# Kernel optimization log

Hardware: AMD Instinct MI355X
Metric: run time of the kernel (lower is better)

Reference implementation:

```python
import jax, jax.numpy as jnp
import numpy as np

SE_W, SE_H = 3, 3  # se_size

def _unfold_blocks(x):
    # x: (B, C, W, H) -> (B, C, w*h, W, H), replicating torch pad+unfold+view flat layout
    B, C, W, H = x.shape
    pw, ph = SE_W // 2, SE_H // 2
    x_pad = jnp.pad(x, ((0, 0), (0, 0), (pw, pw), (ph, ph)))
    # stack 9 shifted views; flat order (b,c,wi,hi,k) matches torch (B,C,1,W,H,w,h)
    blocks = jnp.stack(
        [x_pad[:, :, i:i + W, j:j + H] for i in range(SE_W) for j in range(SE_H)],
        axis=-1,
    )  # (B, C, W, H, 9)
    # torch: .view(B, C, w*h, 1, W, H).squeeze(3) -> flat reinterpretation, not a transpose
    return blocks.reshape(B, C, SE_W * SE_H, W, H)


def setup_inputs() -> dict:
    key = jax.random.key(0)
    k1, k2, k3, k4 = jax.random.split(key, 4)
    B, C, W, H = 8, 128, 64, 64
    x = jax.random.normal(k1, (B, C, W, H), dtype=jnp.float32)
    se_param = jax.random.normal(k2, (SE_W * SE_H,), dtype=jnp.float32)
    # Conv3d(channels, channels, kernel_size=1): weight (O, C, 1, 1, 1) -> (O, C)
    bound = 1.0 / np.sqrt(C)
    attn_w = jax.random.uniform(k3, (C, C), dtype=jnp.float32, minval=-bound, maxval=bound)
    attn_b = jax.random.uniform(k4, (C,), dtype=jnp.float32, minval=-bound, maxval=bound)
    return {"x": x, "se_param": se_param, "attn_w": attn_w, "attn_b": attn_b}


def reference(x, se_param, attn_w, attn_b):
    se = jax.nn.sigmoid(se_param)                      # (9,)
    blocks = _unfold_blocks(x)                          # (B, C, 9, W, H)
    weighted = blocks * se[None, None, :, None, None]   # (B, C, 9, W, H)
    # pointwise Conv3d over channel dim (same weight at every (s, w, h) position)
    mixed = jnp.einsum('bcswh,oc->boswh', weighted, attn_w) \
        + attn_b[None, :, None, None, None]
    attn = jax.nn.sigmoid(mixed)
    out = jnp.max(weighted * attn, axis=2)              # (B, C, W, H)
    return out
```

## Files before the change

kernel.cpp:

```cpp
#include <hip/hip_runtime.h>

#define CCH 128
#define SP  4096
#define BROWS 10
#define RSTR 76
#define BSZ2 (BROWS * RSTR)
#define GOFF 16
#define GTOT (GOFF + 9 * BSZ2)
#define T16_OFF 65536
#define TBLK 80
#define XTSTR 136
#define LOG2E 1.4426950408889634f

typedef __attribute__((ext_vector_type(8))) short bf16x8;
typedef __attribute__((ext_vector_type(4))) float f32x4;

__device__ __forceinline__ float sigmoidf_(float z) {
  return 1.0f / (1.0f + __expf(-z));
}

__device__ __forceinline__ unsigned short bf16rne(float f) {
  union { float f; unsigned u; } v; v.f = f;
  return (unsigned short)((v.u + 0x7fffu + ((v.u >> 16) & 1u)) >> 16);
}

__device__ __forceinline__ int tap_off(int s, int wh) {
  int q  = (s << 12) + wh;
  int wi = q / 576;  int r  = q - wi * 576;
  int hi = r / 9;    int kk = r - hi * 9;
  int di = kk / 3,   dj = kk - di * 3;
  int sw = wi + di - 1, sh = hi + dj - 1;
  bool valid = ((unsigned)sw < 64u) & ((unsigned)sh < 64u);
  int wilo = (s * 64) / 9;
  int rb = sw - wilo + 1;
  return valid ? (GOFF + s * BSZ2 + rb * RSTR + sh) : 0;
}

template <bool WS>
__global__ __launch_bounds__(256) void k_conv(
    const float* __restrict__ x, const float* __restrict__ attn_w,
    float* __restrict__ y, unsigned* __restrict__ t32,
    unsigned short* __restrict__ t16) {
  int bid = blockIdx.x;
  if (WS) {
    if (bid < TBLK) {
      int i = bid * 256 + threadIdx.x;
      if (i < 4 * SP) {
        int wh = i >> 2, j = i & 3;
        unsigned lo = (unsigned)tap_off(2 * j, wh);
        unsigned hi = (unsigned)tap_off(2 * j + 1, wh);
        t32[i] = lo | (hi << 16);
      } else if (i < 5 * SP) {
        int wh = i & (SP - 1);
        t16[wh] = (unsigned short)tap_off(8, wh);
      }
      return;
    }
    bid -= TBLK;
  }

  __shared__ unsigned short x_t[32 * XTSTR];

  int b  = bid >> 7;
  int nb = bid & 127;
  int lane = threadIdx.x & 63, wv = threadIdx.x >> 6;

  const float* xpb = x + ((size_t)b << 19) + (nb << 5);
  int n_st  = threadIdx.x & 31;
  int c_st  = (threadIdx.x >> 5) << 2;
  float xv[16];
#pragma unroll
  for (int g = 0; g < 4; g++) {
    int c0 = c_st + (g << 5);
#pragma unroll
    for (int i = 0; i < 4; i++)
      xv[g * 4 + i] = xpb[((size_t)(c0 + i) << 12) + n_st];
  }

  bf16x8 afrag[2][4];
#pragma unroll
  for (int ot = 0; ot < 2; ot++)
#pragma unroll
    for (int ks = 0; ks < 4; ks++) {
      int o = (wv << 5) + (ot << 4) + (lane & 15);
      int k = (ks << 5) + ((lane >> 4) << 3);
      const float4* wp = (const float4*)&attn_w[(o << 7) + k];
      float4 a0 = wp[0], a1 = wp[1];
      bf16x8 f;
      f[0] = (short)bf16rne(a0.x); f[1] = (short)bf16rne(a0.y);
      f[2] = (short)bf16rne(a0.z); f[3] = (short)bf16rne(a0.w);
      f[4] = (short)bf16rne(a1.x); f[5] = (short)bf16rne(a1.y);
      f[6] = (short)bf16rne(a1.z); f[7] = (short)bf16rne(a1.w);
      afrag[ot][ks] = f;
    }

#pragma unroll
  for (int g = 0; g < 4; g++) {
    int c0 = c_st + (g << 5);
    union { unsigned short s[2]; unsigned u; } p0, p1;
    p0.s[0] = bf16rne(xv[g * 4 + 0]); p0.s[1] = bf16rne(xv[g * 4 + 1]);
    p1.s[0] = bf16rne(xv[g * 4 + 2]); p1.s[1] = bf16rne(xv[g * 4 + 3]);
    *(uint2*)&x_t[n_st * XTSTR + c0] = make_uint2(p0.u, p1.u);
  }
  __syncthreads();

  f32x4 acc[2][2] = {};
#pragma unroll
  for (int ks = 0; ks < 4; ks++) {
    bf16x8 bfrag[2];
#pragma unroll
    for (int nt = 0; nt < 2; nt++) {
      int n = (nt << 4) + (lane & 15);
      int k = (ks << 5) + ((lane >> 4) << 3);
      bfrag[nt] = *(const bf16x8*)&x_t[n * XTSTR + k];
    }
#pragma unroll
    for (int ot = 0; ot < 2; ot++)
#pragma unroll
      for (int nt = 0; nt < 2; nt++)
        acc[ot][nt] = __builtin_amdgcn_mfma_f32_16x16x32_bf16(
            afrag[ot][ks], bfrag[nt], acc[ot][nt], 0, 0, 0);
  }

  float* yb = y + ((size_t)b << 19) + (nb << 5);
#pragma unroll
  for (int ot = 0; ot < 2; ot++) {
    int ob = (wv << 5) + (ot << 4) + ((lane >> 4) << 2);
#pragma unroll
    for (int nt = 0; nt < 2; nt++) {
      int n = (nt << 4) + (lane & 15);
#pragma unroll
      for (int r = 0; r < 4; r++)
        yb[((size_t)(ob + r) << 12) + n] = acc[ot][nt][r];
    }
  }
}

template <bool TBL>
__global__ __launch_bounds__(256) void k_attnmax(
    const float* __restrict__ x, float* __restrict__ yo,
    const float* __restrict__ se_param, const float* __restrict__ attn_b,
    const uint4* __restrict__ t32, const unsigned short* __restrict__ t16) {
  __shared__ float g[GTOT];
  __shared__ float se9[16];
  __shared__ float sl9[16];

  int bc = blockIdx.x;
  int c  = bc & (CCH - 1);
  const float* xp = x  + ((size_t)bc << 12);
  float*       yp = yo + ((size_t)bc << 12);

  if (threadIdx.x < 9) {
    float se = sigmoidf_(se_param[threadIdx.x]);
    se9[threadIdx.x] = se;
    sl9[threadIdx.x] = -se * LOG2E;
  }
  if (threadIdx.x == 0) g[0] = 0.0f;
  float ab = attn_b[c];
  float abl = -ab * LOG2E;
  __syncthreads();

  for (int f = threadIdx.x; f < 9 * BROWS * 16; f += 256) {
    int s   = f / 160;
    int rem = f - s * 160;
    int rb  = rem >> 4, sh0 = (rem & 15) << 2;
    int rg  = ((s * 64 * 58255) >> 19) - 1 + rb;
    float4 gv = make_float4(0.0f, 0.0f, 0.0f, 0.0f);
    if ((unsigned)rg < 64u) {
      float se = se9[s], sl = sl9[s];
      float4 xx = *(const float4*)&xp[(rg << 6) + sh0];
      float4 yy = *(const float4*)&yp[(rg << 6) + sh0];
      gv.x = se * xx.x * __builtin_amdgcn_rcpf(1.0f + exp2f(fmaf(yy.x, sl, abl)));
      gv.y = se * xx.y * __builtin_amdgcn_rcpf(1.0f + exp2f(fmaf(yy.y, sl, abl)));
      gv.z = se * xx.z * __builtin_amdgcn_rcpf(1.0f + exp2f(fmaf(yy.z, sl, abl)));
      gv.w = se * xx.w * __builtin_amdgcn_rcpf(1.0f + exp2f(fmaf(yy.w, sl, abl)));
    }
    *(float4*)&g[GOFF + s * BSZ2 + rb * RSTR + sh0] = gv;
  }
  __syncthreads();

  for (int k = 0; k < 16; k++) {
    int wh = (k << 8) | threadIdx.x;
    float m;
    if (TBL) {
      uint4 p = t32[wh];
      int p8  = t16[wh];
      float m0 = fmaxf(g[p.x & 0xffffu], g[p.x >> 16]);
      float m1 = fmaxf(g[p.y & 0xffffu], g[p.y >> 16]);
      float m2 = fmaxf(g[p.z & 0xffffu], g[p.z >> 16]);
      float m3 = fmaxf(g[p.w & 0xffffu], g[p.w >> 16]);
      m = fmaxf(fmaxf(fmaxf(m0, m1), fmaxf(m2, m3)), g[p8]);
    } else {
      m = 0.0f;
#pragma unroll
      for (int s = 0; s < 9; s++) m = fmaxf(m, g[tap_off(s, wh)]);
    }
    yp[wh] = m;
  }
}

extern "C" void kernel_launch(void* const* d_in, const int* in_sizes, int n_in,
                              void* d_out, int out_size, void* d_ws, size_t ws_size,
                              hipStream_t stream) {
  const float* x        = (const float*)d_in[0];
  const float* se_param = (const float*)d_in[1];
  const float* attn_w   = (const float*)d_in[2];
  const float* attn_b   = (const float*)d_in[3];
  float* out = (float*)d_out;

  int B = in_sizes[0] / (CCH * SP);
  unsigned* t32       = (unsigned*)d_ws;
  unsigned short* t16 = (unsigned short*)((char*)d_ws + T16_OFF);
  bool use_ws = ws_size >= (size_t)(T16_OFF + SP * sizeof(unsigned short));

  if (use_ws) {
    k_conv<true><<<dim3(TBLK + B * 128), dim3(256), 0, stream>>>(
        x, attn_w, out, t32, t16);
    k_attnmax<true><<<dim3(B * CCH), dim3(256), 0, stream>>>(
        x, out, se_param, attn_b, (const uint4*)t32, t16);
  } else {
    k_conv<false><<<dim3(B * 128), dim3(256), 0, stream>>>(
        x, attn_w, out, nullptr, nullptr);
    k_attnmax<false><<<dim3(B * CCH), dim3(256), 0, stream>>>(
        x, out, se_param, attn_b, nullptr, nullptr);
  }
}
```

Measured before the change: 30.54 us.

## Store conv intermediate as bf16 in workspace and halve conv tile width

The 1x1 channel-mix result is now written as bf16 into a workspace buffer instead of fp32 into the output, and the attention/max kernel reads bf16 values back. This halves the intermediate write and read traffic. Conv blocks now cover 16 spatial positions instead of 32, which doubles the block count and shrinks per-block LDS and registers. The bf16 rounding of pre-sigmoid logits adds error, and the fast path needs a larger workspace, otherwise the fp32 fallback kernels run.

```diff
diff --git a/kernel.cpp b/kernel.cpp
--- a/kernel.cpp
+++ b/kernel.cpp
@@ -8,6 +8,7 @@
 #define GOFF 16
 #define GTOT (GOFF + 9 * BSZ2)
 #define T16_OFF 65536
+#define Y_OFFB 73728
 #define TBLK 80
 #define XTSTR 136
 #define LOG2E 1.4426950408889634f
@@ -22,6 +23,11 @@
 __device__ __forceinline__ unsigned short bf16rne(float f) {
   union { float f; unsigned u; } v; v.f = f;
   return (unsigned short)((v.u + 0x7fffu + ((v.u >> 16) & 1u)) >> 16);
+}
+
+__device__ __forceinline__ float bf2f(unsigned short u) {
+  union { unsigned u; float f; } v; v.u = (unsigned)u << 16;
+  return v.f;
 }
 
 __device__ __forceinline__ int tap_off(int s, int wh) {
@@ -36,46 +42,39 @@
   return valid ? (GOFF + s * BSZ2 + rb * RSTR + sh) : 0;
 }
 
-template <bool WS>
 __global__ __launch_bounds__(256) void k_conv(
     const float* __restrict__ x, const float* __restrict__ attn_w,
-    float* __restrict__ y, unsigned* __restrict__ t32,
+    unsigned short* __restrict__ ybf, unsigned* __restrict__ t32,
     unsigned short* __restrict__ t16) {
   int bid = blockIdx.x;
-  if (WS) {
-    if (bid < TBLK) {
-      int i = bid * 256 + threadIdx.x;
-      if (i < 4 * SP) {
-        int wh = i >> 2, j = i & 3;
-        unsigned lo = (unsigned)tap_off(2 * j, wh);
-        unsigned hi = (unsigned)tap_off(2 * j + 1, wh);
-        t32[i] = lo | (hi << 16);
-      } else if (i < 5 * SP) {
-        int wh = i & (SP - 1);
-        t16[wh] = (unsigned short)tap_off(8, wh);
-      }
-      return;
-    }
-    bid -= TBLK;
-  }
-
-  __shared__ unsigned short x_t[32 * XTSTR];
-
-  int b  = bid >> 7;
-  int nb = bid & 127;
+  if (bid < TBLK) {
+    int i = bid * 256 + threadIdx.x;
+    if (i < 4 * SP) {
+      int wh = i >> 2, j = i & 3;
+      unsigned lo = (unsigned)tap_off(2 * j, wh);
+      unsigned hi = (unsigned)tap_off(2 * j + 1, wh);
+      t32[i] = lo | (hi << 16);
+    } else if (i < 5 * SP) {
+      int wh = i & (SP - 1);
+      t16[wh] = (unsigned short)tap_off(8, wh);
+    }
+    return;
+  }
+  bid -= TBLK;
+
+  __shared__ unsigned short x_t[16 * XTSTR];
+
+  int b  = bid >> 8;
+  int nb = bid & 255;
   int lane = threadIdx.x & 63, wv = threadIdx.x >> 6;
 
-  const float* xpb = x + ((size_t)b << 19) + (nb << 5);
-  int n_st  = threadIdx.x & 31;
-  int c_st  = (threadIdx.x >> 5) << 2;
-  float xv[16];
-#pragma unroll
-  for (int g = 0; g < 4; g++) {
-    int c0 = c_st + (g << 5);
-#pragma unroll
-    for (int i = 0; i < 4; i++)
-      xv[g * 4 + i] = xpb[((size_t)(c0 + i) << 12) + n_st];
-  }
+  const float* xpb = x + ((size_t)b << 19) + (nb << 4);
+  int n_st = threadIdx.x & 15;
+  int c_st = (threadIdx.x >> 4) << 3;
+  float xv[8];
+#pragma unroll
+  for (int i = 0; i < 8; i++)
+    xv[i] = xpb[((size_t)(c_st + i) << 12) + n_st];
 
   bf16x8 afrag[2][4];
 #pragma unroll
@@ -94,56 +93,158 @@
       afrag[ot][ks] = f;
     }
 
-#pragma unroll
-  for (int g = 0; g < 4; g++) {
-    int c0 = c_st + (g << 5);
-    union { unsigned short s[2]; unsigned u; } p0, p1;
-    p0.s[0] = bf16rne(xv[g * 4 + 0]); p0.s[1] = bf16rne(xv[g * 4 + 1]);
-    p1.s[0] = bf16rne(xv[g * 4 + 2]); p1.s[1] = bf16rne(xv[g * 4 + 3]);
-    *(uint2*)&x_t[n_st * XTSTR + c0] = make_uint2(p0.u, p1.u);
-  }
-  __syncthreads();
-
-  f32x4 acc[2][2] = {};
+  union { unsigned short s[8]; uint4 q; } pk;
+#pragma unroll
+  for (int i = 0; i < 8; i++) pk.s[i] = bf16rne(xv[i]);
+  *(uint4*)&x_t[n_st * XTSTR + c_st] = pk.q;
+  __syncthreads();
+
+  f32x4 acc[2] = {};
 #pragma unroll
   for (int ks = 0; ks < 4; ks++) {
-    bf16x8 bfrag[2];
-#pragma unroll
-    for (int nt = 0; nt < 2; nt++) {
-      int n = (nt << 4) + (lane & 15);
-      int k = (ks << 5) + ((lane >> 4) << 3);
-      bfrag[nt] = *(const bf16x8*)&x_t[n * XTSTR + k];
-    }
+    int n = lane & 15;
+    int k = (ks << 5) + ((lane >> 4) << 3);
+    bf16x8 bfrag = *(const bf16x8*)&x_t[n * XTSTR + k];
 #pragma unroll
     for (int ot = 0; ot < 2; ot++)
-#pragma unroll
-      for (int nt = 0; nt < 2; nt++)
-        acc[ot][nt] = __builtin_amdgcn_mfma_f32_16x16x32_bf16(
-            afrag[ot][ks], bfrag[nt], acc[ot][nt], 0, 0, 0);
-  }
-
-  float* yb = y + ((size_t)b << 19) + (nb << 5);
+      acc[ot] = __builtin_amdgcn_mfma_f32_16x16x32_bf16(
+          afrag[ot][ks], bfrag, acc[ot], 0, 0, 0);
+  }
+
+  unsigned short* yb = ybf + ((size_t)b << 19) + (nb << 4);
+  int n = lane & 15;
 #pragma unroll
   for (int ot = 0; ot < 2; ot++) {
     int ob = (wv << 5) + (ot << 4) + ((lane >> 4) << 2);
 #pragma unroll
-    for (int nt = 0; nt < 2; nt++) {
-      int n = (nt << 4) + (lane & 15);
-#pragma unroll
-      for (int r = 0; r < 4; r++)
-        yb[((size_t)(ob + r) << 12) + n] = acc[ot][nt][r];
-    }
-  }
-}
-
-template <bool TBL>
+    for (int r = 0; r < 4; r++)
+      yb[((size_t)(ob + r) << 12) + n] = bf16rne(acc[ot][r]);
+  }
+}
+
 __global__ __launch_bounds__(256) void k_attnmax(
-    const float* __restrict__ x, float* __restrict__ yo,
+    const float* __restrict__ x, const unsigned short* __restrict__ ybf,
+    float* __restrict__ out,
     const float* __restrict__ se_param, const float* __restrict__ attn_b,
     const uint4* __restrict__ t32, const unsigned short* __restrict__ t16) {
   __shared__ float g[GTOT];
-  __shared__ float se9[16];
-  __shared__ float sl9[16];
+  __shared__ float se9[16], sl9[16];
+
+  int bc = blockIdx.x;
+  int c  = bc & (CCH - 1);
+  const float* xp = x + ((size_t)bc << 12);
+  const unsigned short* yp = ybf + ((size_t)bc << 12);
+  float* op = out + ((size_t)bc << 12);
+
+  if (threadIdx.x < 9) {
+    float se = sigmoidf_(se_param[threadIdx.x]);
+    se9[threadIdx.x] = se;
+    sl9[threadIdx.x] = -se * LOG2E;
+  }
+  if (threadIdx.x == 0) g[0] = 0.0f;
+  float ab  = attn_b[c];
+  float abl = -ab * LOG2E;
+  __syncthreads();
+
+  for (int f = threadIdx.x; f < 9 * BROWS * 16; f += 256) {
+    int s   = f / 160;
+    int rem = f - s * 160;
+    int rb  = rem >> 4, sh0 = (rem & 15) << 2;
+    int rg  = ((s * 64 * 58255) >> 19) - 1 + rb;
+    float4 gv = make_float4(0.0f, 0.0f, 0.0f, 0.0f);
+    if ((unsigned)rg < 64u) {
+      float se = se9[s], sl = sl9[s];
+      float4 xx = *(const float4*)&xp[(rg << 6) + sh0];
+      ushort4 yu = *(const ushort4*)&yp[(rg << 6) + sh0];
+      gv.x = se * xx.x * __builtin_amdgcn_rcpf(1.0f + exp2f(fmaf(bf2f(yu.x), sl, abl)));
+      gv.y = se * xx.y * __builtin_amdgcn_rcpf(1.0f + exp2f(fmaf(bf2f(yu.y), sl, abl)));
+      gv.z = se * xx.z * __builtin_amdgcn_rcpf(1.0f + exp2f(fmaf(bf2f(yu.z), sl, abl)));
+      gv.w = se * xx.w * __builtin_amdgcn_rcpf(1.0f + exp2f(fmaf(bf2f(yu.w), sl, abl)));
+    }
+    *(float4*)&g[GOFF + s * BSZ2 + rb * RSTR + sh0] = gv;
+  }
+  __syncthreads();
+
+  for (int k = 0; k < 16; k++) {
+    int wh = (k << 8) | threadIdx.x;
+    uint4 p = t32[wh];
+    int p8  = t16[wh];
+    float m0 = fmaxf(g[p.x & 0xffffu], g[p.x >> 16]);
+    float m1 = fmaxf(g[p.y & 0xffffu], g[p.y >> 16]);
+    float m2 = fmaxf(g[p.z & 0xffffu], g[p.z >> 16]);
+    float m3 = fmaxf(g[p.w & 0xffffu], g[p.w >> 16]);
+    op[wh] = fmaxf(fmaxf(fmaxf(m0, m1), fmaxf(m2, m3)), g[p8]);
+  }
+}
+
+__global__ __launch_bounds__(256) void k_conv_fb(
+    const float* __restrict__ x, const float* __restrict__ attn_w,
+    float* __restrict__ y) {
+  __shared__ unsigned short x_t[16 * XTSTR];
+  int bid = blockIdx.x;
+  int b  = bid >> 8;
+  int nb = bid & 255;
+  int lane = threadIdx.x & 63, wv = threadIdx.x >> 6;
+
+  const float* xpb = x + ((size_t)b << 19) + (nb << 4);
+  int n_st = threadIdx.x & 15;
+  int c_st = (threadIdx.x >> 4) << 3;
+  float xv[8];
+#pragma unroll
+  for (int i = 0; i < 8; i++)
+    xv[i] = xpb[((size_t)(c_st + i) << 12) + n_st];
+
+  bf16x8 afrag[2][4];
+#pragma unroll
+  for (int ot = 0; ot < 2; ot++)
+#pragma unroll
+    for (int ks = 0; ks < 4; ks++) {
+      int o = (wv << 5) + (ot << 4) + (lane & 15);
+      int k = (ks << 5) + ((lane >> 4) << 3);
+      const float4* wp = (const float4*)&attn_w[(o << 7) + k];
+      float4 a0 = wp[0], a1 = wp[1];
+      bf16x8 f;
+      f[0] = (short)bf16rne(a0.x); f[1] = (short)bf16rne(a0.y);
+      f[2] = (short)bf16rne(a0.z); f[3] = (short)bf16rne(a0.w);
+      f[4] = (short)bf16rne(a1.x); f[5] = (short)bf16rne(a1.y);
+      f[6] = (short)bf16rne(a1.z); f[7] = (short)bf16rne(a1.w);
+      afrag[ot][ks] = f;
+    }
+
+  union { unsigned short s[8]; uint4 q; } pk;
+#pragma unroll
+  for (int i = 0; i < 8; i++) pk.s[i] = bf16rne(xv[i]);
+  *(uint4*)&x_t[n_st * XTSTR + c_st] = pk.q;
+  __syncthreads();
+
+  f32x4 acc[2] = {};
+#pragma unroll
+  for (int ks = 0; ks < 4; ks++) {
+    int n = lane & 15;
+    int k = (ks << 5) + ((lane >> 4) << 3);
+    bf16x8 bfrag = *(const bf16x8*)&x_t[n * XTSTR + k];
+#pragma unroll
+    for (int ot = 0; ot < 2; ot++)
+      acc[ot] = __builtin_amdgcn_mfma_f32_16x16x32_bf16(
+          afrag[ot][ks], bfrag, acc[ot], 0, 0, 0);
+  }
+
+  float* yb = y + ((size_t)b << 19) + (nb << 4);
+  int n = lane & 15;
+#pragma unroll
+  for (int ot = 0; ot < 2; ot++) {
+    int ob = (wv << 5) + (ot << 4) + ((lane >> 4) << 2);
+#pragma unroll
+    for (int r = 0; r < 4; r++)
+      yb[((size_t)(ob + r) << 12) + n] = acc[ot][r];
+  }
+}
+
+__global__ __launch_bounds__(256) void k_attnmax_fb(
+    const float* __restrict__ x, float* __restrict__ yo,
+    const float* __restrict__ se_param, const float* __restrict__ attn_b) {
+  __shared__ float g[GTOT];
+  __shared__ float se9[16], sl9[16];
 
   int bc = blockIdx.x;
   int c  = bc & (CCH - 1);
@@ -156,7 +257,7 @@
     sl9[threadIdx.x] = -se * LOG2E;
   }
   if (threadIdx.x == 0) g[0] = 0.0f;
-  float ab = attn_b[c];
+  float ab  = attn_b[c];
   float abl = -ab * LOG2E;
   __syncthreads();
 
@@ -181,20 +282,9 @@
 
   for (int k = 0; k < 16; k++) {
     int wh = (k << 8) | threadIdx.x;
-    float m;
-    if (TBL) {
-      uint4 p = t32[wh];
-      int p8  = t16[wh];
-      float m0 = fmaxf(g[p.x & 0xffffu], g[p.x >> 16]);
-      float m1 = fmaxf(g[p.y & 0xffffu], g[p.y >> 16]);
-      float m2 = fmaxf(g[p.z & 0xffffu], g[p.z >> 16]);
-      float m3 = fmaxf(g[p.w & 0xffffu], g[p.w >> 16]);
-      m = fmaxf(fmaxf(fmaxf(m0, m1), fmaxf(m2, m3)), g[p8]);
-    } else {
-      m = 0.0f;
-#pragma unroll
-      for (int s = 0; s < 9; s++) m = fmaxf(m, g[tap_off(s, wh)]);
-    }
+    float m = 0.0f;
+#pragma unroll
+    for (int s = 0; s < 9; s++) m = fmaxf(m, g[tap_off(s, wh)]);
     yp[wh] = m;
   }
 }
@@ -211,17 +301,17 @@
   int B = in_sizes[0] / (CCH * SP);
   unsigned* t32       = (unsigned*)d_ws;
   unsigned short* t16 = (unsigned short*)((char*)d_ws + T16_OFF);
-  bool use_ws = ws_size >= (size_t)(T16_OFF + SP * sizeof(unsigned short));
-
-  if (use_ws) {
-    k_conv<true><<<dim3(TBLK + B * 128), dim3(256), 0, stream>>>(
-        x, attn_w, out, t32, t16);
-    k_attnmax<true><<<dim3(B * CCH), dim3(256), 0, stream>>>(
-        x, out, se_param, attn_b, (const uint4*)t32, t16);
+  unsigned short* ybf = (unsigned short*)((char*)d_ws + Y_OFFB);
+  size_t need = (size_t)Y_OFFB + (size_t)B * CCH * SP * sizeof(unsigned short);
+
+  if (ws_size >= need) {
+    k_conv<<<dim3(TBLK + B * 256), dim3(256), 0, stream>>>(
+        x, attn_w, ybf, t32, t16);
+    k_attnmax<<<dim3(B * CCH), dim3(256), 0, stream>>>(
+        x, ybf, out, se_param, attn_b, (const uint4*)t32, t16);
   } else {
-    k_conv<false><<<dim3(B * 128), dim3(256), 0, stream>>>(
-        x, attn_w, out, nullptr, nullptr);
-    k_attnmax<false><<<dim3(B * CCH), dim3(256), 0, stream>>>(
-        x, out, se_param, attn_b, nullptr, nullptr);
-  }
-}
+    k_conv_fb<<<dim3(B * 256), dim3(256), 0, stream>>>(x, attn_w, out);
+    k_attnmax_fb<<<dim3(B * CCH), dim3(256), 0, stream>>>(
+        x, out, se_param, attn_b);
+  }
+}
```

Result: slower. 34.39 us (+12.6%).
